# Kernel optimization log

Hardware: AMD Instinct MI355X
Metric: run time of the kernel (lower is better)

Reference implementation:

```python
import jax, jax.numpy as jnp
import numpy as np

SIM_THRESHOLD = 0.5   # similarity_threshold
LAMBDA = 0.1          # lambda_weight default


def setup_inputs() -> dict:
    key = jax.random.key(0)
    ks = jax.random.split(key, 8)
    B, T, C, P = 8, 1024, 1024, 100
    return {
        "attention_scores": jax.random.normal(ks[0], (B, T, T), jnp.float32),
        "context": jax.random.normal(ks[1], (B, C), jnp.float32),
        "triggers": jax.random.normal(ks[2], (P, C), jnp.float32),
        "biases": jax.random.uniform(ks[3], (P, T, T), jnp.float32),
        "confidences": jnp.ones((P,), jnp.float32),
        "W1": jax.random.normal(ks[4], (2 * C, C), jnp.float32) * (1.0 / np.sqrt(2 * C)),
        "b1": jnp.zeros((C,), jnp.float32),
        "W2": jax.random.normal(ks[5], (C,), jnp.float32) * (1.0 / np.sqrt(C)),
        "b2": jnp.zeros((1,), jnp.float32),
    }


def reference(attention_scores, context, triggers, biases, confidences, W1, b1, W2, b2):
    C = context.shape[-1]
    # combined = cat([context, trigger]) @ W1 == context @ W1[:C] + trigger @ W1[C:]
    ctx_h = context @ W1[:C]              # (B, C)
    trg_h = triggers @ W1[C:]             # (P, C)
    h = jax.nn.relu(ctx_h[:, None, :] + trg_h[None, :, :] + b1)   # (B, P, C)
    logits = h @ W2 + b2[0]               # (B, P)
    scores = jax.nn.sigmoid(logits).mean(axis=0)                  # (P,) mean over batch
    # match: only patterns with score > threshold contribute, weighted by score*confidence
    weights = jnp.where(scores > SIM_THRESHOLD, scores * confidences, 0.0)  # (P,)
    reasoning_bias = jnp.einsum("p,pij->ij", weights, biases)     # (T, T)
    return attention_scores + LAMBDA * reasoning_bias[None, :, :]
```

## Files before the change

kernel.cpp:

```cpp
#include <hip/hip_runtime.h>
#include <hip/hip_bf16.h>
#include <math.h>

#define BD 8
#define TD 1024
#define CD 1024
#define PD 100
#define KS 16
#define KW (CD / KS)
#define SEG 2048
#define LAMBDA 0.1f
#define SIM_THR 0.5f

typedef float f4 __attribute__((ext_vector_type(4)));

__device__ float    g_pctx[KS][BD][CD];
__device__ float    g_ptrg[KS][PD][CD];
__device__ float    g_wd[PD];
__device__ float    g_wc[PD];
__device__ unsigned g_poff[PD];
__device__ int      g_nnz;

__global__ __launch_bounds__(256) void hidden_kernel(const float* __restrict__ context,
                                                     const float* __restrict__ triggers,
                                                     const float* __restrict__ W1) {
    const int c  = blockIdx.x * 256 + threadIdx.x;
    const int kz = blockIdx.z;
    const int k0 = kz * KW;
    const bool is_ctx = (blockIdx.y == 0);
    const int  ych = blockIdx.y - 1;
    const float* __restrict__ W1p = is_ctx ? W1 : (W1 + (size_t)CD * CD);
    const float* __restrict__ src = is_ctx ? context : (triggers + (size_t)ych * 10 * CD);
    float* __restrict__ dst = is_ctx ? &g_pctx[kz][0][0] : &g_ptrg[kz][ych * 10][0];
    const int nrows = is_ctx ? 8 : 10;

    __shared__ float s_src[10][KW];
    for (int t = threadIdx.x; t < 10 * KW; t += 256) {
        const int r = t >> 6, k = t & (KW - 1);
        s_src[r][k] = src[(size_t)(r < nrows ? r : 0) * CD + k0 + k];
    }
    __syncthreads();

    float acc[10];
#pragma unroll
    for (int i = 0; i < 10; ++i) acc[i] = 0.f;

#pragma unroll 8
    for (int kk = 0; kk < KW; ++kk) {
        const float wv = W1p[(size_t)(k0 + kk) * CD + c];
#pragma unroll
        for (int i = 0; i < 10; ++i)
            acc[i] = fmaf(s_src[i][kk], wv, acc[i]);
    }
#pragma unroll
    for (int i = 0; i < 10; ++i)
        if (i < nrows) dst[(size_t)i * CD + c] = acc[i];
}

__global__ __launch_bounds__(512) void score_kernel(const float* __restrict__ b1,
                                                    const float* __restrict__ W2,
                                                    const float* __restrict__ b2,
                                                    const float* __restrict__ conf) {
    const int p = blockIdx.x;
    __shared__ float s_h[CD];
    __shared__ float s_logit[BD];

    for (int c = threadIdx.x; c < CD; c += 512) {
        float v = b1[c];
#pragma unroll
        for (int kz = 0; kz < KS; ++kz) v += g_ptrg[kz][p][c];
        s_h[c] = v;
    }
    __syncthreads();

    const int b = threadIdx.x >> 6, lane = threadIdx.x & 63;
    float sum = 0.f;
    for (int c = lane; c < CD; c += 64) {
        float v = s_h[c];
#pragma unroll
        for (int kz = 0; kz < KS; ++kz) v += g_pctx[kz][b][c];
        sum = fmaf(fmaxf(v, 0.f), W2[c], sum);
    }
#pragma unroll
    for (int off = 32; off > 0; off >>= 1) sum += __shfl_down(sum, off);
    if (lane == 0) s_logit[b] = sum + b2[0];
    __syncthreads();
    if (threadIdx.x == 0) {
        float s = 0.f;
#pragma unroll
        for (int bb = 0; bb < BD; ++bb) s += 1.f / (1.f + expf(-s_logit[bb]));
        s *= (1.f / BD);
        g_wd[p] = (s > SIM_THR) ? s * conf[p] * LAMBDA : 0.f;
    }
}

__global__ void compact_kernel() {
    if (threadIdx.x == 0) {
        int n = 0;
        for (int q = 0; q < PD; ++q) {
            const float w = g_wd[q];
            if (w != 0.f) {
                g_wc[n]   = w;
                g_poff[n] = (unsigned)(q * (TD * TD));
                ++n;
            }
        }
        g_nnz = n;
    }
}

__global__ __launch_bounds__(256) void out_kernel(const float* __restrict__ attn,
                                                  const float* __restrict__ biases,
                                                  float* __restrict__ out) {
    __shared__ float    s_w[PD];
    __shared__ unsigned s_off[PD];
    __shared__ float    s_part[4][SEG];
    const int n = g_nnz;
    if (threadIdx.x < n) {
        s_w[threadIdx.x]   = g_wc[threadIdx.x];
        s_off[threadIdx.x] = g_poff[threadIdx.x];
    }
    __syncthreads();

    const int wv = threadIdx.x >> 6, lane = threadIdx.x & 63;
    const size_t seg = (size_t)blockIdx.x * SEG;

    f4 acc[8];
#pragma unroll
    for (int j = 0; j < 8; ++j) acc[j] = (f4){0.f, 0.f, 0.f, 0.f};

    for (int t = wv; t < n; t += 4) {
        const float w = s_w[t];
        const float* bp = biases + (size_t)s_off[t] + seg + (size_t)lane * 4;
        f4 v[8];
#pragma unroll
        for (int j = 0; j < 8; ++j) v[j] = *(const f4*)(bp + j * 256);
#pragma unroll
        for (int j = 0; j < 8; ++j) {
            acc[j].x = fmaf(w, v[j].x, acc[j].x);
            acc[j].y = fmaf(w, v[j].y, acc[j].y);
            acc[j].z = fmaf(w, v[j].z, acc[j].z);
            acc[j].w = fmaf(w, v[j].w, acc[j].w);
        }
    }

#pragma unroll
    for (int j = 0; j < 8; ++j)
        *(f4*)&s_part[wv][j * 256 + lane * 4] = acc[j];
    __syncthreads();

    const int e = threadIdx.x * 8;
    f4 r0 = (f4){0.f, 0.f, 0.f, 0.f}, r1 = r0;
#pragma unroll
    for (int w2 = 0; w2 < 4; ++w2) {
        r0 += *(const f4*)&s_part[w2][e];
        r1 += *(const f4*)&s_part[w2][e + 4];
    }

#pragma unroll
    for (int b = 0; b < BD; ++b) {
        const size_t off = (size_t)b * TD * TD + seg + (size_t)e;
        const f4 a0 = *(const f4*)(attn + off);
        const f4 a1 = *(const f4*)(attn + off + 4);
        __builtin_nontemporal_store(a0 + r0, (f4*)(out + off));
        __builtin_nontemporal_store(a1 + r1, (f4*)(out + off + 4));
    }
}

extern "C" void kernel_launch(void* const* d_in, const int* in_sizes, int n_in,
                              void* d_out, int out_size, void* d_ws, size_t ws_size,
                              hipStream_t stream) {
    const float* attn     = (const float*)d_in[0];
    const float* context  = (const float*)d_in[1];
    const float* triggers = (const float*)d_in[2];
    const float* biases   = (const float*)d_in[3];
    const float* conf     = (const float*)d_in[4];
    const float* W1       = (const float*)d_in[5];
    const float* b1       = (const float*)d_in[6];
    const float* W2       = (const float*)d_in[7];
    const float* b2       = (const float*)d_in[8];
    float* out = (float*)d_out;

    hipLaunchKernelGGL(hidden_kernel, dim3(CD / 256, 11, KS), dim3(256), 0, stream,
                       context, triggers, W1);
    hipLaunchKernelGGL(score_kernel, dim3(PD), dim3(512), 0, stream, b1, W2, b2, conf);
    hipLaunchKernelGGL(compact_kernel, dim3(1), dim3(64), 0, stream);
    hipLaunchKernelGGL(out_kernel, dim3(TD * TD / SEG), dim3(256), 0, stream, attn, biases, out);
}
```

Before: 111.1 us.

## Fold compaction into out kernel, presum context partials, split cached/nontemporal bias loads

Removes the single-thread compact kernel and rebuilds the nonzero pattern list inside each out_kernel block with wave ballots and popcounts. Adds a small ctxsum kernel that reduces the context partial sums once, instead of having every score block redo the 16-way reduction for all batches. In the bias accumulation, patterns at index SPLITQ or above are read with nontemporal loads so that only part of the bias tensor competes for cache. Each out block now does extra per-block compaction work, and the SPLITQ split is a heuristic chosen for cache residency.

Measured after the change: 103.0 us. -7.3%, faster.

```diff
diff --git a/kernel.cpp b/kernel.cpp
--- a/kernel.cpp
+++ b/kernel.cpp
@@ -9,17 +9,17 @@
 #define KS 16
 #define KW (CD / KS)
 #define SEG 2048
+#define TT (TD * TD)
+#define SPLITQ 48
 #define LAMBDA 0.1f
 #define SIM_THR 0.5f
 
 typedef float f4 __attribute__((ext_vector_type(4)));
 
-__device__ float    g_pctx[KS][BD][CD];
-__device__ float    g_ptrg[KS][PD][CD];
-__device__ float    g_wd[PD];
-__device__ float    g_wc[PD];
-__device__ unsigned g_poff[PD];
-__device__ int      g_nnz;
+__device__ float g_pctx[KS][BD][CD];
+__device__ float g_ptrg[KS][PD][CD];
+__device__ float g_ctxb[BD][CD];
+__device__ float g_wd[PD];
 
 __global__ __launch_bounds__(256) void hidden_kernel(const float* __restrict__ context,
                                                      const float* __restrict__ triggers,
@@ -57,8 +57,16 @@
         if (i < nrows) dst[(size_t)i * CD + c] = acc[i];
 }
 
-__global__ __launch_bounds__(512) void score_kernel(const float* __restrict__ b1,
-                                                    const float* __restrict__ W2,
+__global__ __launch_bounds__(256) void ctxsum_kernel(const float* __restrict__ b1) {
+    const int idx = blockIdx.x * 256 + threadIdx.x;
+    const int b = idx >> 10, c = idx & (CD - 1);
+    float v = b1[c];
+#pragma unroll
+    for (int kz = 0; kz < KS; ++kz) v += g_pctx[kz][b][c];
+    g_ctxb[b][c] = v;
+}
+
+__global__ __launch_bounds__(512) void score_kernel(const float* __restrict__ W2,
                                                     const float* __restrict__ b2,
                                                     const float* __restrict__ conf) {
     const int p = blockIdx.x;
@@ -66,7 +74,7 @@
     __shared__ float s_logit[BD];
 
     for (int c = threadIdx.x; c < CD; c += 512) {
-        float v = b1[c];
+        float v = 0.f;
 #pragma unroll
         for (int kz = 0; kz < KS; ++kz) v += g_ptrg[kz][p][c];
         s_h[c] = v;
@@ -76,9 +84,7 @@
     const int b = threadIdx.x >> 6, lane = threadIdx.x & 63;
     float sum = 0.f;
     for (int c = lane; c < CD; c += 64) {
-        float v = s_h[c];
-#pragma unroll
-        for (int kz = 0; kz < KS; ++kz) v += g_pctx[kz][b][c];
+        const float v = s_h[c] + g_ctxb[b][c];
         sum = fmaf(fmaxf(v, 0.f), W2[c], sum);
     }
 #pragma unroll
@@ -91,21 +97,6 @@
         for (int bb = 0; bb < BD; ++bb) s += 1.f / (1.f + expf(-s_logit[bb]));
         s *= (1.f / BD);
         g_wd[p] = (s > SIM_THR) ? s * conf[p] * LAMBDA : 0.f;
-    }
-}
-
-__global__ void compact_kernel() {
-    if (threadIdx.x == 0) {
-        int n = 0;
-        for (int q = 0; q < PD; ++q) {
-            const float w = g_wd[q];
-            if (w != 0.f) {
-                g_wc[n]   = w;
-                g_poff[n] = (unsigned)(q * (TD * TD));
-                ++n;
-            }
-        }
-        g_nnz = n;
     }
 }
 
@@ -114,13 +105,29 @@
                                                   float* __restrict__ out) {
     __shared__ float    s_w[PD];
     __shared__ unsigned s_off[PD];
+    __shared__ int      s_n;
     __shared__ float    s_part[4][SEG];
-    const int n = g_nnz;
-    if (threadIdx.x < n) {
-        s_w[threadIdx.x]   = g_wc[threadIdx.x];
-        s_off[threadIdx.x] = g_poff[threadIdx.x];
-    }
-    __syncthreads();
+
+    if (threadIdx.x < 64) {
+        const int lane = threadIdx.x;
+        const float w0 = g_wd[lane];
+        const float w1 = (lane < PD - 64) ? g_wd[lane + 64] : 0.f;
+        const unsigned long long m0 = __ballot(w0 != 0.f);
+        const unsigned long long m1 = __ballot(w1 != 0.f);
+        const unsigned long long below = (1ull << lane) - 1;
+        const int c0 = __popcll(m0);
+        if (w0 != 0.f) {
+            const int i = __popcll(m0 & below);
+            s_w[i] = w0; s_off[i] = (unsigned)(lane * TT);
+        }
+        if (w1 != 0.f) {
+            const int i = c0 + __popcll(m1 & below);
+            s_w[i] = w1; s_off[i] = (unsigned)((lane + 64) * TT);
+        }
+        if (lane == 0) s_n = c0 + __popcll(m1);
+    }
+    __syncthreads();
+    const int n = s_n;
 
     const int wv = threadIdx.x >> 6, lane = threadIdx.x & 63;
     const size_t seg = (size_t)blockIdx.x * SEG;
@@ -133,8 +140,14 @@
         const float w = s_w[t];
         const float* bp = biases + (size_t)s_off[t] + seg + (size_t)lane * 4;
         f4 v[8];
-#pragma unroll
-        for (int j = 0; j < 8; ++j) v[j] = *(const f4*)(bp + j * 256);
+        if (s_off[t] < (unsigned)(SPLITQ * TT)) {
+#pragma unroll
+            for (int j = 0; j < 8; ++j) v[j] = *(const f4*)(bp + j * 256);
+        } else {
+#pragma unroll
+            for (int j = 0; j < 8; ++j)
+                v[j] = __builtin_nontemporal_load((const f4*)(bp + j * 256));
+        }
 #pragma unroll
         for (int j = 0; j < 8; ++j) {
             acc[j].x = fmaf(w, v[j].x, acc[j].x);
@@ -159,7 +172,7 @@
 
 #pragma unroll
     for (int b = 0; b < BD; ++b) {
-        const size_t off = (size_t)b * TD * TD + seg + (size_t)e;
+        const size_t off = (size_t)b * TT + seg + (size_t)e;
         const f4 a0 = *(const f4*)(attn + off);
         const f4 a1 = *(const f4*)(attn + off + 4);
         __builtin_nontemporal_store(a0 + r0, (f4*)(out + off));
@@ -183,7 +196,7 @@
 
     hipLaunchKernelGGL(hidden_kernel, dim3(CD / 256, 11, KS), dim3(256), 0, stream,
                        context, triggers, W1);
-    hipLaunchKernelGGL(score_kernel, dim3(PD), dim3(512), 0, stream, b1, W2, b2, conf);
-    hipLaunchKernelGGL(compact_kernel, dim3(1), dim3(64), 0, stream);
-    hipLaunchKernelGGL(out_kernel, dim3(TD * TD / SEG), dim3(256), 0, stream, attn, biases, out);
-}
+    hipLaunchKernelGGL(ctxsum_kernel, dim3(BD * CD / 256), dim3(256), 0, stream, b1);
+    hipLaunchKernelGGL(score_kernel, dim3(PD), dim3(512), 0, stream, W2, b2, conf);
+    hipLaunchKernelGGL(out_kernel, dim3(TT / SEG), dim3(256), 0, stream, attn, biases, out);
+}
```
